# Kernel tuning notes

Hardware: AMD Instinct MI355X
Metric: run time of the kernel (lower is better)

## Reference

```python
import jax, jax.numpy as jnp
import numpy as np


def _lstm(x_seq, W, U, b, h0, c0):
    """Keras-default LSTM. x_seq: [B,T,F]. Gate order i,f,g,o.
    Returns (all hidden states [B,T,H], final h [B,H], final c [B,H])."""
    H = U.shape[0]
    # precompute input projections for all timesteps: [T,B,4H]
    xz = jnp.einsum('btf,fg->tbg', x_seq, W) + b

    def step(carry, xz_t):
        h, c = carry
        z = xz_t + h @ U  # [B,4H]
        i = jax.nn.sigmoid(z[:, 0 * H:1 * H])
        f = jax.nn.sigmoid(z[:, 1 * H:2 * H])
        g = jnp.tanh(z[:, 2 * H:3 * H])
        o = jax.nn.sigmoid(z[:, 3 * H:4 * H])
        c = f * c + i * g
        h = o * jnp.tanh(c)
        return (h, c), h

    (hT, cT), hs = jax.lax.scan(step, (h0, c0), xz)
    return jnp.transpose(hs, (1, 0, 2)), hT, cT  # [B,T,H], [B,H], [B,H]


def setup_inputs() -> dict:
    key = jax.random.key(0)
    ks = jax.random.split(key, 7)
    B, T, F, H, C = 128, 512, 128, 512, 10
    s_in1 = 1.0 / np.sqrt(F)
    s_h = 1.0 / np.sqrt(H)
    return {
        'x': jax.random.normal(ks[0], (B, T, F), jnp.float32),
        'W1': jax.random.normal(ks[1], (F, 4 * H), jnp.float32) * s_in1,
        'U1': jax.random.normal(ks[2], (H, 4 * H), jnp.float32) * s_h,
        'b1': jnp.zeros((4 * H,), jnp.float32),
        'W2': jax.random.normal(ks[3], (H, 4 * H), jnp.float32) * s_h,
        'U2': jax.random.normal(ks[4], (H, 4 * H), jnp.float32) * s_h,
        'b2': jnp.zeros((4 * H,), jnp.float32),
        'Wd': jax.random.normal(ks[5], (H, C), jnp.float32) * s_h,
        'bd': jnp.zeros((C,), jnp.float32),
    }


def reference(x, W1, U1, b1, W2, U2, b2, Wd, bd):
    B = x.shape[0]
    H = U1.shape[0]
    h0 = jnp.zeros((B, H), x.dtype)
    c0 = jnp.zeros((B, H), x.dtype)
    # lstm1: return_sequences + return_state
    seq, h1, c1 = _lstm(x, W1, U1, b1, h0, c0)
    # Keras RNN called on [seq, h, c] uses (h, c) as lstm2's initial state
    _, h2, _ = _lstm(seq, W2, U2, b2, h1, c1)
    logits = h2 @ Wd + bd
    return jax.nn.softmax(logits, axis=-1)
```

## Files before the change

### kernel.cpp

```cpp
#include <hip/hip_runtime.h>
#include <math.h>

#define BB 128
#define TT 512
#define FF 128
#define HH 512
#define NR 2048
#define HB (HH*BB)

typedef __attribute__((ext_vector_type(8))) short short8;
typedef __attribute__((ext_vector_type(4))) float f32x4;
typedef unsigned int uint;
typedef unsigned short ushort;

#define MFMA __builtin_amdgcn_mfma_f32_16x16x32_bf16

__device__ __forceinline__ ushort f2bf(float f) {
  uint u = __float_as_uint(f);
  u += 0x7fff + ((u >> 16) & 1);
  return (ushort)(u >> 16);
}


__global__ __launch_bounds__(256) void k_zero(float* __restrict__ p, int n) {
  int i = blockIdx.x * 256 + threadIdx.x;
  if (i < n) p[i] = 0.f;
}

__global__ __launch_bounds__(256) void k_rearr_b(const float* __restrict__ src,
                                                 float* __restrict__ dst) {
  int idx = blockIdx.x * 256 + threadIdx.x;
  int j = idx & 511, g = idx >> 9;
  dst[j * 4 + g] = src[idx];
}

__global__ __launch_bounds__(256) void k_pack_A(const float* __restrict__ src,
                                                ushort* __restrict__ dst, int ktsh) {
  int idx = blockIdx.x * 256 + threadIdx.x;
  int KTm1 = (1 << ktsh) - 1;
  int j8 = idx & 7;
  int L = (idx >> 3) & 63;
  int kt = (idx >> 9) & KTm1;
  int jb = idx >> (9 + ktsh);
  int k = kt * 32 + (L >> 4) * 8 + j8;
  int m = L & 15;
  int j = jb * 4 + (m >> 2);
  int g = m & 3;
  float v = src[(size_t)k * NR + g * HH + j];
  ushort hi = f2bf(v);
  float fhi = __uint_as_float(((uint)hi) << 16);
  ushort lo = f2bf(v - fhi);
  size_t base = ((size_t)((jb << ktsh) + kt) * 64 + L) * 16;
  dst[base + j8] = hi;
  dst[base + 8 + j8] = lo;
}

__global__ __launch_bounds__(256, 1) void k_fused(
    const float* __restrict__ x,
    const ushort* __restrict__ W1pk, const ushort* __restrict__ U1pk,
    const float* __restrict__ bp1,
    const ushort* __restrict__ W2pk, const ushort* __restrict__ U2pk,
    const float* __restrict__ bp2,
    uint* __restrict__ seq, uint* __restrict__ ring2,
    int* __restrict__ flags) {
  int tid = threadIdx.x;
  int L = tid & 63;
  int ct = tid >> 6;
  int jb = blockIdx.x >> 1;
  int bh = blockIdx.x & 1;
  int q = L >> 4, n = L & 15;
  int col = bh * 64 + ct * 16 + n;
  int j = jb * 4 + q;
  int hrow = q * 8;
  int fi0 = bh * 128 + L;
  int fi1 = fi0 + 64;
  int fme = bh * 128 + jb;

  short8 uh[16], ul[16];
  short8 w1h[4], w1l[4];
  {
    const ushort* ub = U1pk + ((size_t)(jb * 16) * 64 + L) * 16;
#pragma unroll
    for (int kt = 0; kt < 16; ++kt) {
      uh[kt] = *(const short8*)(ub + kt * 1024);
      ul[kt] = *(const short8*)(ub + kt * 1024 + 8);
    }
    const ushort* wb = W1pk + ((size_t)(jb * 4) * 64 + L) * 16;
#pragma unroll
    for (int kt = 0; kt < 4; ++kt) {
      w1h[kt] = *(const short8*)(wb + kt * 1024);
      w1l[kt] = *(const short8*)(wb + kt * 1024 + 8);
    }
  }
  float4 bv = *(const float4*)(bp1 + j * 4);
  float c_reg = 0.f;
  const float* xb = x + (size_t)col * (TT * FF) + hrow;

  f32x4 a0 = {0.f, 0.f, 0.f, 0.f}, a1 = a0, a2 = a0;

#define XPROJ(S) { \
    const float* xp = xb + (size_t)(S) * FF; \
    _Pragma("unroll") \
    for (int kt = 0; kt < 4; ++kt) { \
      float4 v0 = *(const float4*)(xp + kt * 32); \
      float4 v1 = *(const float4*)(xp + kt * 32 + 4); \
      float xf[8] = {v0.x, v0.y, v0.z, v0.w, v1.x, v1.y, v1.z, v1.w}; \
      short8 bhi, blo; \
      _Pragma("unroll") \
      for (int u = 0; u < 8; ++u) { \
        ushort hi = f2bf(xf[u]); \
        blo[u] = (short)f2bf(xf[u] - __uint_as_float(((uint)hi) << 16)); \
        bhi[u] = (short)hi; \
      } \
      a0 = MFMA(w1h[kt], bhi, a0, 0, 0, 0); \
      a1 = MFMA(w1l[kt], bhi, a1, 0, 0, 0); \
      a2 = MFMA(w1h[kt], blo, a2, 0, 0, 0); \
    } }

#define POLL(TGT) { \
    while (true) { \
      int f0 = __hip_atomic_load(&flags[fi0], __ATOMIC_RELAXED, __HIP_MEMORY_SCOPE_AGENT); \
      int f1 = __hip_atomic_load(&flags[fi1], __ATOMIC_RELAXED, __HIP_MEMORY_SCOPE_AGENT); \
      if (__all((f0 >= (TGT)) && (f1 >= (TGT)))) break; \
    } \
    asm volatile("" ::: "memory"); }

  XPROJ(0)
#pragma unroll 1
  for (int s = 0; s < TT; ++s) {
    if (s > 0) {
      POLL(s)
      const uint* hc = seq + (size_t)(s - 1) * HB + (size_t)hrow * BB + col;
      uint w[16][8];
#pragma unroll
      for (int kt = 0; kt < 16; ++kt)
#pragma unroll
        for (int u = 0; u < 8; ++u)
          w[kt][u] = hc[(size_t)(kt * 32 + u) * BB];
#pragma unroll
      for (int kt = 0; kt < 16; ++kt) {
        short8 bhi, blo;
#pragma unroll
        for (int u = 0; u < 8; ++u) {
          bhi[u] = (short)(w[kt][u] >> 16);
          blo[u] = (short)(w[kt][u] & 0xffffu);
        }
        a0 = MFMA(uh[kt], bhi, a0, 0, 0, 0);
        a1 = MFMA(ul[kt], bhi, a1, 0, 0, 0);
        a2 = MFMA(uh[kt], blo, a2, 0, 0, 0);
      }
    }
    float z0 = a0.x + a1.x + a2.x + bv.x;
    float z1 = a0.y + a1.y + a2.y + bv.y;
    float z2 = a0.z + a1.z + a2.z + bv.z;
    float z3 = a0.w + a1.w + a2.w + bv.w;
    float ig = 1.f / (1.f + __expf(-z0));
    float fg = 1.f / (1.f + __expf(-z1));
    float gg = tanhf(z2);
    float og = 1.f / (1.f + __expf(-z3));
    c_reg = fg * c_reg + ig * gg;
    float hn = og * tanhf(c_reg);
    ushort hi = f2bf(hn);
    uint word = (((uint)hi) << 16) |
                (uint)f2bf(hn - __uint_as_float(((uint)hi) << 16));
    __hip_atomic_store(&seq[(size_t)s * HB + (size_t)j * BB + col], word,
                       __ATOMIC_RELAXED, __HIP_MEMORY_SCOPE_AGENT);
    if (s == TT - 1)
      __hip_atomic_store(&ring2[(size_t)3 * HB + (size_t)j * BB + col], word,
                         __ATOMIC_RELAXED, __HIP_MEMORY_SCOPE_AGENT);
    __syncthreads();
    if (tid == 0)
      __hip_atomic_store(&flags[fme], s + 1, __ATOMIC_RELAXED,
                         __HIP_MEMORY_SCOPE_AGENT);
    a0 = (f32x4){0.f, 0.f, 0.f, 0.f}; a1 = a0; a2 = a0;
    if (s + 1 < TT) XPROJ(s + 1)
  }

  {
    const ushort* ub = U2pk + ((size_t)(jb * 16) * 64 + L) * 16;
#pragma unroll
    for (int kt = 0; kt < 16; ++kt) {
      uh[kt] = *(const short8*)(ub + kt * 1024);
      ul[kt] = *(const short8*)(ub + kt * 1024 + 8);
    }
  }
  bv = *(const float4*)(bp2 + j * 4);
  const ushort* w2b = W2pk + ((size_t)(jb * 16) * 64 + L) * 16;

#define G1PROJ(S) { \
    const uint* h1c = seq + (size_t)(S) * HB + (size_t)hrow * BB + col; \
    uint w[16][8]; \
    _Pragma("unroll") \
    for (int kt = 0; kt < 16; ++kt) \
      _Pragma("unroll") \
      for (int u = 0; u < 8; ++u) \
        w[kt][u] = h1c[(size_t)(kt * 32 + u) * BB]; \
    _Pragma("unroll") \
    for (int kt = 0; kt < 16; ++kt) { \
      short8 w2h = *(const short8*)(w2b + kt * 1024); \
      short8 w2l = *(const short8*)(w2b + kt * 1024 + 8); \
      short8 bhi, blo; \
      _Pragma("unroll") \
      for (int u = 0; u < 8; ++u) { \
        bhi[u] = (short)(w[kt][u] >> 16); \
        blo[u] = (short)(w[kt][u] & 0xffffu); \
      } \
      a0 = MFMA(w2h, bhi, a0, 0, 0, 0); \
      a1 = MFMA(w2l, bhi, a1, 0, 0, 0); \
      a2 = MFMA(w2h, blo, a2, 0, 0, 0); \
    } }

  G1PROJ(0)
#pragma unroll 1
  for (int s = 0; s < TT; ++s) {
    POLL(TT + s)
    {
      const uint* hc = ring2 + (size_t)((s + 3) & 3) * HB + (size_t)hrow * BB + col;
      uint w[16][8];
#pragma unroll
      for (int kt = 0; kt < 16; ++kt)
#pragma unroll
        for (int u = 0; u < 8; ++u)
          w[kt][u] = __hip_atomic_load(&hc[(size_t)(kt * 32 + u) * BB],
                                       __ATOMIC_RELAXED, __HIP_MEMORY_SCOPE_AGENT);
#pragma unroll
      for (int kt = 0; kt < 16; ++kt) {
        short8 bhi, blo;
#pragma unroll
        for (int u = 0; u < 8; ++u) {
          bhi[u] = (short)(w[kt][u] >> 16);
          blo[u] = (short)(w[kt][u] & 0xffffu);
        }
        a0 = MFMA(uh[kt], bhi, a0, 0, 0, 0);
        a1 = MFMA(ul[kt], bhi, a1, 0, 0, 0);
        a2 = MFMA(uh[kt], blo, a2, 0, 0, 0);
      }
    }
    float z0 = a0.x + a1.x + a2.x + bv.x;
    float z1 = a0.y + a1.y + a2.y + bv.y;
    float z2 = a0.z + a1.z + a2.z + bv.z;
    float z3 = a0.w + a1.w + a2.w + bv.w;
    float ig = 1.f / (1.f + __expf(-z0));
    float fg = 1.f / (1.f + __expf(-z1));
    float gg = tanhf(z2);
    float og = 1.f / (1.f + __expf(-z3));
    c_reg = fg * c_reg + ig * gg;
    float hn = og * tanhf(c_reg);
    ushort hi = f2bf(hn);
    uint word = (((uint)hi) << 16) |
                (uint)f2bf(hn - __uint_as_float(((uint)hi) << 16));
    __hip_atomic_store(&ring2[(size_t)(s & 3) * HB + (size_t)j * BB + col], word,
                       __ATOMIC_RELAXED, __HIP_MEMORY_SCOPE_AGENT);
    __syncthreads();
    if (tid == 0)
      __hip_atomic_store(&flags[fme], TT + s + 1, __ATOMIC_RELAXED,
                         __HIP_MEMORY_SCOPE_AGENT);
    a0 = (f32x4){0.f, 0.f, 0.f, 0.f}; a1 = a0; a2 = a0;
    if (s + 1 < TT) G1PROJ(s + 1)
  }
}

__global__ __launch_bounds__(64) void k_dense(const uint* __restrict__ h2,
                                              const float* __restrict__ Wd,
                                              const float* __restrict__ bd,
                                              float* __restrict__ out) {
  int b = blockIdx.x * 64 + threadIdx.x;
  float acc[10];
#pragma unroll
  for (int c = 0; c < 10; ++c) acc[c] = bd[c];
  for (int k = 0; k < HH; ++k) {
    uint w = h2[k * BB + b];
    float hv = __uint_as_float(w & 0xffff0000u) + __uint_as_float(w << 16);
#pragma unroll
    for (int c = 0; c < 10; ++c) acc[c] = fmaf(hv, Wd[k * 10 + c], acc[c]);
  }
  float m = acc[0];
#pragma unroll
  for (int c = 1; c < 10; ++c) m = fmaxf(m, acc[c]);
  float s = 0.f;
#pragma unroll
  for (int c = 0; c < 10; ++c) { acc[c] = __expf(acc[c] - m); s += acc[c]; }
  float inv = 1.f / s;
#pragma unroll
  for (int c = 0; c < 10; ++c) out[b * 10 + c] = acc[c] * inv;
}

extern "C" void kernel_launch(void* const* d_in, const int* in_sizes, int n_in,
                              void* d_out, int out_size, void* d_ws, size_t ws_size,
                              hipStream_t stream) {
  const float* x  = (const float*)d_in[0];
  const float* W1 = (const float*)d_in[1];
  const float* U1 = (const float*)d_in[2];
  const float* b1 = (const float*)d_in[3];
  const float* W2 = (const float*)d_in[4];
  const float* U2 = (const float*)d_in[5];
  const float* b2 = (const float*)d_in[6];
  const float* Wd = (const float*)d_in[7];
  const float* bd = (const float*)d_in[8];
  float* out = (float*)d_out;

  uint*   seq   = (uint*)d_ws;
  uint*   ring2 = seq + (size_t)TT * HB;
  float*  bp1   = (float*)(ring2 + (size_t)4 * HB);
  float*  bp2   = bp1 + NR;
  ushort* W1pk  = (ushort*)(bp2 + NR);
  ushort* U1pk  = W1pk + (size_t)524288;
  ushort* U2pk  = U1pk + (size_t)2097152;
  ushort* W2pk  = U2pk + (size_t)2097152;
  int*    flags = (int*)(W2pk + (size_t)2097152);

  k_zero<<<1, 256, 0, stream>>>((float*)flags, 256);
  k_rearr_b<<<NR / 256, 256, 0, stream>>>(b1, bp1);
  k_rearr_b<<<NR / 256, 256, 0, stream>>>(b2, bp2);
  k_pack_A<<<1024, 256, 0, stream>>>(W1, W1pk, 2);
  k_pack_A<<<4096, 256, 0, stream>>>(U1, U1pk, 4);
  k_pack_A<<<4096, 256, 0, stream>>>(U2, U2pk, 4);
  k_pack_A<<<4096, 256, 0, stream>>>(W2, W2pk, 4);

  k_fused<<<256, 256, 0, stream>>>(x, W1pk, U1pk, bp1, W2pk, U2pk, bp2,
                                   seq, ring2, flags);
  k_dense<<<BB / 64, 64, 0, stream>>>(ring2 + (size_t)3 * HB, Wd, bd, out);
}
```

Measured before the change: 5.088 ms.

## Split persistent LSTM kernel into recurrent and input-projection block roles

The 256 persistent blocks are split into two roles. 128 recurrent blocks each own two hidden-row tiles for 32 batch columns and run only the h@U recurrence across both layers. The other 128 blocks compute the input projections (x@W1, then h1@W2) up to four steps ahead into a ring buffer, with producer/consumer flags padded onto separate cache lines. The hidden state is now stored as separate hi/lo bf16 planes in batch-major layout, so operand fetches are contiguous 16-byte loads instead of strided 32-bit gathers. This takes the projection work off the serial critical path, at the cost of holding twice as many U registers per recurrent block and adding a second synchronisation channel.

Measured after the change: 8.399 ms. 65.1% more time.

```diff
diff --git a/kernel.cpp b/kernel.cpp
--- a/kernel.cpp
+++ b/kernel.cpp
@@ -7,18 +7,29 @@
 #define HH 512
 #define NR 2048
 #define HB (HH*BB)
+#define FLS 16
 
 typedef __attribute__((ext_vector_type(8))) short short8;
 typedef __attribute__((ext_vector_type(4))) float f32x4;
 typedef unsigned int uint;
 typedef unsigned short ushort;
+typedef unsigned long long u64;
 
 #define MFMA __builtin_amdgcn_mfma_f32_16x16x32_bf16
+#define AT_LD(p)   __hip_atomic_load((p), __ATOMIC_RELAXED, __HIP_MEMORY_SCOPE_AGENT)
+#define AT_ST(p,v) __hip_atomic_store((p), (v), __ATOMIC_RELAXED, __HIP_MEMORY_SCOPE_AGENT)
 
 __device__ __forceinline__ ushort f2bf(float f) {
   uint u = __float_as_uint(f);
   u += 0x7fff + ((u >> 16) & 1);
   return (ushort)(u >> 16);
+}
+__device__ __forceinline__ float bfh(ushort h) { return __uint_as_float(((uint)h) << 16); }
+__device__ __forceinline__ void st2_wt(ushort* p, uint v) {
+  asm volatile("global_store_short %0, %1, off sc0 sc1" :: "v"(p), "v"(v) : "memory");
+}
+__device__ __forceinline__ u64 pk2f(float a, float b) {
+  return ((u64)__float_as_uint(b) << 32) | (u64)__float_as_uint(a);
 }
 
 
@@ -48,8 +59,7 @@
   int g = m & 3;
   float v = src[(size_t)k * NR + g * HH + j];
   ushort hi = f2bf(v);
-  float fhi = __uint_as_float(((uint)hi) << 16);
-  ushort lo = f2bf(v - fhi);
+  ushort lo = f2bf(v - bfh(hi));
   size_t base = ((size_t)((jb << ktsh) + kt) * 64 + L) * 16;
   dst[base + j8] = hi;
   dst[base + 8 + j8] = lo;
@@ -61,206 +71,234 @@
     const float* __restrict__ bp1,
     const ushort* __restrict__ W2pk, const ushort* __restrict__ U2pk,
     const float* __restrict__ bp2,
-    uint* __restrict__ seq, uint* __restrict__ ring2,
-    int* __restrict__ flags) {
+    ushort* __restrict__ shi, ushort* __restrict__ slo,
+    ushort* __restrict__ rhi, ushort* __restrict__ rlo,
+    float4* __restrict__ xzr,
+    int* __restrict__ hflags, int* __restrict__ pflags) {
   int tid = threadIdx.x;
   int L = tid & 63;
-  int ct = tid >> 6;
-  int jb = blockIdx.x >> 1;
-  int bh = blockIdx.x & 1;
+  int w = tid >> 6;
   int q = L >> 4, n = L & 15;
-  int col = bh * 64 + ct * 16 + n;
-  int j = jb * 4 + q;
-  int hrow = q * 8;
-  int fi0 = bh * 128 + L;
-  int fi1 = fi0 + 64;
-  int fme = bh * 128 + jb;
-
-  short8 uh[16], ul[16];
-  short8 w1h[4], w1l[4];
-  {
-    const ushort* ub = U1pk + ((size_t)(jb * 16) * 64 + L) * 16;
-#pragma unroll
-    for (int kt = 0; kt < 16; ++kt) {
-      uh[kt] = *(const short8*)(ub + kt * 1024);
-      ul[kt] = *(const short8*)(ub + kt * 1024 + 8);
+  int rtp = w & 1, ctw = w >> 1;
+  bool isrec = (blockIdx.x < 128);
+  int b = isrec ? blockIdx.x : (blockIdx.x - 128);
+  int ch = b & 3, jb2 = b >> 2;
+  int col = ch * 32 + ctw * 16 + n;
+  int jbp0 = jb2 * 4 + rtp * 2;
+  int j0 = jbp0 * 4 + q;
+
+  if (isrec) {
+    short8 uh[2][16], ul[2][16];
+    auto loadU = [&](const ushort* Up) {
+#pragma unroll
+      for (int r = 0; r < 2; ++r)
+#pragma unroll
+        for (int kt = 0; kt < 16; ++kt) {
+          const ushort* p = Up + (((size_t)(jbp0 + r) * 16 + kt) * 64 + L) * 16;
+          uh[r][kt] = *(const short8*)(p);
+          ul[r][kt] = *(const short8*)(p + 8);
+        }
+    };
+    loadU(U1pk);
+    float4 bv[2];
+    bv[0] = *(const float4*)(bp1 + j0 * 4);
+    bv[1] = *(const float4*)(bp1 + (j0 + 4) * 4);
+    float c_reg[2] = {0.f, 0.f};
+    int fidx = ((L & 31) * 4 + ch) * FLS;
+
+#pragma unroll 1
+    for (int G = 0; G < 2 * TT; ++G) {
+      if (G == TT) {
+        loadU(U2pk);
+        bv[0] = *(const float4*)(bp2 + j0 * 4);
+        bv[1] = *(const float4*)(bp2 + (j0 + 4) * 4);
+      }
+      while (true) {
+        int hf = AT_LD(hflags + fidx);
+        int pf = AT_LD(pflags + b * FLS);
+        if (__all((hf >= G) && (pf >= G + 1))) break;
+      }
+      asm volatile("" ::: "memory");
+      float xzv[2][4];
+#pragma unroll
+      for (int r = 0; r < 2; ++r) {
+        const u64* xp = (const u64*)(xzr + ((size_t)(G & 3) * HB + (j0 + 4 * r) * BB + col));
+        u64 a = AT_LD(xp), bq = AT_LD(xp + 1);
+        xzv[r][0] = __uint_as_float((uint)a);
+        xzv[r][1] = __uint_as_float((uint)(a >> 32));
+        xzv[r][2] = __uint_as_float((uint)bq);
+        xzv[r][3] = __uint_as_float((uint)(bq >> 32));
+      }
+      f32x4 A0[2], A1[2], A2[2];
+#pragma unroll
+      for (int r = 0; r < 2; ++r) {
+        A0[r] = (f32x4){0.f, 0.f, 0.f, 0.f}; A1[r] = A0[r]; A2[r] = A0[r];
+      }
+      if (G != 0) {
+        if (G < TT) {
+          const ushort* ph = shi + (size_t)(G - 1) * HB + (size_t)col * HH + q * 8;
+          const ushort* pl = slo + (size_t)(G - 1) * HB + (size_t)col * HH + q * 8;
+#pragma unroll
+          for (int kh = 0; kh < 2; ++kh) {
+            short8 bh[8], bl[8];
+#pragma unroll
+            for (int k8 = 0; k8 < 8; ++k8) {
+              bh[k8] = *(const short8*)(ph + (kh * 8 + k8) * 32);
+              bl[k8] = *(const short8*)(pl + (kh * 8 + k8) * 32);
+            }
+#pragma unroll
+            for (int k8 = 0; k8 < 8; ++k8) {
+              int kt = kh * 8 + k8;
+#pragma unroll
+              for (int r = 0; r < 2; ++r) {
+                A0[r] = MFMA(uh[r][kt], bh[k8], A0[r], 0, 0, 0);
+                A1[r] = MFMA(ul[r][kt], bh[k8], A1[r], 0, 0, 0);
+                A2[r] = MFMA(uh[r][kt], bl[k8], A2[r], 0, 0, 0);
+              }
+            }
+          }
+        } else {
+          size_t rb = (size_t)((G - 1) & 3) * HB + (size_t)col * HH + q * 8;
+          const u64* ph = (const u64*)(rhi + rb);
+          const u64* pl = (const u64*)(rlo + rb);
+#pragma unroll
+          for (int kh = 0; kh < 2; ++kh) {
+            short8 bh[8], bl[8];
+#pragma unroll
+            for (int k8 = 0; k8 < 8; ++k8) {
+              int kt = kh * 8 + k8;
+              union { short8 v; u64 u[2]; } fh, fl;
+              fh.u[0] = AT_LD(ph + kt * 8); fh.u[1] = AT_LD(ph + kt * 8 + 1);
+              fl.u[0] = AT_LD(pl + kt * 8); fl.u[1] = AT_LD(pl + kt * 8 + 1);
+              bh[k8] = fh.v; bl[k8] = fl.v;
+            }
+#pragma unroll
+            for (int k8 = 0; k8 < 8; ++k8) {
+              int kt = kh * 8 + k8;
+#pragma unroll
+              for (int r = 0; r < 2; ++r) {
+                A0[r] = MFMA(uh[r][kt], bh[k8], A0[r], 0, 0, 0);
+                A1[r] = MFMA(ul[r][kt], bh[k8], A1[r], 0, 0, 0);
+                A2[r] = MFMA(uh[r][kt], bl[k8], A2[r], 0, 0, 0);
+              }
+            }
+          }
+        }
+      }
+#pragma unroll
+      for (int r = 0; r < 2; ++r) {
+        float z0 = A0[r].x + A1[r].x + A2[r].x + xzv[r][0];
+        float z1 = A0[r].y + A1[r].y + A2[r].y + xzv[r][1];
+        float z2 = A0[r].z + A1[r].z + A2[r].z + xzv[r][2];
+        float z3 = A0[r].w + A1[r].w + A2[r].w + xzv[r][3];
+        float ig = 1.f / (1.f + __expf(-z0));
+        float fg = 1.f / (1.f + __expf(-z1));
+        float gg = tanhf(z2);
+        float og = 1.f / (1.f + __expf(-z3));
+        c_reg[r] = fg * c_reg[r] + ig * gg;
+        float hn = og * tanhf(c_reg[r]);
+        ushort hh = f2bf(hn);
+        ushort hl = f2bf(hn - bfh(hh));
+        size_t off = (size_t)col * HH + (j0 + 4 * r);
+        if (G < TT) {
+          st2_wt(shi + (size_t)G * HB + off, hh);
+          st2_wt(slo + (size_t)G * HB + off, hl);
+        }
+        if (G >= TT - 1) {
+          st2_wt(rhi + (size_t)(G & 3) * HB + off, hh);
+          st2_wt(rlo + (size_t)(G & 3) * HB + off, hl);
+        }
+      }
+      __syncthreads();
+      if (tid == 0) AT_ST(hflags + b * FLS, G + 1);
     }
-    const ushort* wb = W1pk + ((size_t)(jb * 4) * 64 + L) * 16;
-#pragma unroll
-    for (int kt = 0; kt < 4; ++kt) {
-      w1h[kt] = *(const short8*)(wb + kt * 1024);
-      w1l[kt] = *(const short8*)(wb + kt * 1024 + 8);
+  } else {
+    short8 w1h[2][4], w1l[2][4];
+#pragma unroll
+    for (int r = 0; r < 2; ++r)
+#pragma unroll
+      for (int kt = 0; kt < 4; ++kt) {
+        const ushort* p = W1pk + (((size_t)(jbp0 + r) * 4 + kt) * 64 + L) * 16;
+        w1h[r][kt] = *(const short8*)(p);
+        w1l[r][kt] = *(const short8*)(p + 8);
+      }
+    float4 bv[2];
+    bv[0] = *(const float4*)(bp1 + j0 * 4);
+    bv[1] = *(const float4*)(bp1 + (j0 + 4) * 4);
+
+#pragma unroll 1
+    for (int G = 0; G < 2 * TT; ++G) {
+      if (G == TT) {
+        bv[0] = *(const float4*)(bp2 + j0 * 4);
+        bv[1] = *(const float4*)(bp2 + (j0 + 4) * 4);
+      }
+      if (G >= 4) {
+        while (AT_LD(hflags + b * FLS) < G - 3) {}
+      }
+      asm volatile("" ::: "memory");
+      f32x4 P0[2], P1[2], P2[2];
+#pragma unroll
+      for (int r = 0; r < 2; ++r) {
+        P0[r] = (f32x4){0.f, 0.f, 0.f, 0.f}; P1[r] = P0[r]; P2[r] = P0[r];
+      }
+      if (G < TT) {
+        const float* xp = x + ((size_t)col * TT + G) * FF + q * 8;
+#pragma unroll
+        for (int kt = 0; kt < 4; ++kt) {
+          float4 v0 = *(const float4*)(xp + kt * 32);
+          float4 v1 = *(const float4*)(xp + kt * 32 + 4);
+          float xf[8] = {v0.x, v0.y, v0.z, v0.w, v1.x, v1.y, v1.z, v1.w};
+          short8 xh, xl;
+#pragma unroll
+          for (int u = 0; u < 8; ++u) {
+            ushort hi = f2bf(xf[u]);
+            xl[u] = (short)f2bf(xf[u] - bfh(hi));
+            xh[u] = (short)hi;
+          }
+#pragma unroll
+          for (int r = 0; r < 2; ++r) {
+            P0[r] = MFMA(w1h[r][kt], xh, P0[r], 0, 0, 0);
+            P1[r] = MFMA(w1l[r][kt], xh, P1[r], 0, 0, 0);
+            P2[r] = MFMA(w1h[r][kt], xl, P2[r], 0, 0, 0);
+          }
+        }
+      } else {
+        int sp = G - TT;
+        const ushort* ph = shi + (size_t)sp * HB + (size_t)col * HH + q * 8;
+        const ushort* pl = slo + (size_t)sp * HB + (size_t)col * HH + q * 8;
+#pragma unroll
+        for (int kt = 0; kt < 16; ++kt) {
+          short8 bh = *(const short8*)(ph + kt * 32);
+          short8 bl = *(const short8*)(pl + kt * 32);
+#pragma unroll
+          for (int r = 0; r < 2; ++r) {
+            const ushort* ab = W2pk + (((size_t)(jbp0 + r) * 16 + kt) * 64 + L) * 16;
+            short8 ah = *(const short8*)(ab);
+            short8 al = *(const short8*)(ab + 8);
+            P0[r] = MFMA(ah, bh, P0[r], 0, 0, 0);
+            P1[r] = MFMA(al, bh, P1[r], 0, 0, 0);
+            P2[r] = MFMA(ah, bl, P2[r], 0, 0, 0);
+          }
+        }
+      }
+#pragma unroll
+      for (int r = 0; r < 2; ++r) {
+        float o0 = P0[r].x + P1[r].x + P2[r].x + bv[r].x;
+        float o1 = P0[r].y + P1[r].y + P2[r].y + bv[r].y;
+        float o2 = P0[r].z + P1[r].z + P2[r].z + bv[r].z;
+        float o3 = P0[r].w + P1[r].w + P2[r].w + bv[r].w;
+        u64* dp = (u64*)(xzr + ((size_t)(G & 3) * HB + (j0 + 4 * r) * BB + col));
+        AT_ST(dp, pk2f(o0, o1));
+        AT_ST(dp + 1, pk2f(o2, o3));
+      }
+      __syncthreads();
+      if (tid == 0) AT_ST(pflags + b * FLS, G + 1);
     }
   }
-  float4 bv = *(const float4*)(bp1 + j * 4);
-  float c_reg = 0.f;
-  const float* xb = x + (size_t)col * (TT * FF) + hrow;
-
-  f32x4 a0 = {0.f, 0.f, 0.f, 0.f}, a1 = a0, a2 = a0;
-
-#define XPROJ(S) { \
-    const float* xp = xb + (size_t)(S) * FF; \
-    _Pragma("unroll") \
-    for (int kt = 0; kt < 4; ++kt) { \
-      float4 v0 = *(const float4*)(xp + kt * 32); \
-      float4 v1 = *(const float4*)(xp + kt * 32 + 4); \
-      float xf[8] = {v0.x, v0.y, v0.z, v0.w, v1.x, v1.y, v1.z, v1.w}; \
-      short8 bhi, blo; \
-      _Pragma("unroll") \
-      for (int u = 0; u < 8; ++u) { \
-        ushort hi = f2bf(xf[u]); \
-        blo[u] = (short)f2bf(xf[u] - __uint_as_float(((uint)hi) << 16)); \
-        bhi[u] = (short)hi; \
-      } \
-      a0 = MFMA(w1h[kt], bhi, a0, 0, 0, 0); \
-      a1 = MFMA(w1l[kt], bhi, a1, 0, 0, 0); \
-      a2 = MFMA(w1h[kt], blo, a2, 0, 0, 0); \
-    } }
-
-#define POLL(TGT) { \
-    while (true) { \
-      int f0 = __hip_atomic_load(&flags[fi0], __ATOMIC_RELAXED, __HIP_MEMORY_SCOPE_AGENT); \
-      int f1 = __hip_atomic_load(&flags[fi1], __ATOMIC_RELAXED, __HIP_MEMORY_SCOPE_AGENT); \
-      if (__all((f0 >= (TGT)) && (f1 >= (TGT)))) break; \
-    } \
-    asm volatile("" ::: "memory"); }
-
-  XPROJ(0)
-#pragma unroll 1
-  for (int s = 0; s < TT; ++s) {
-    if (s > 0) {
-      POLL(s)
-      const uint* hc = seq + (size_t)(s - 1) * HB + (size_t)hrow * BB + col;
-      uint w[16][8];
-#pragma unroll
-      for (int kt = 0; kt < 16; ++kt)
-#pragma unroll
-        for (int u = 0; u < 8; ++u)
-          w[kt][u] = hc[(size_t)(kt * 32 + u) * BB];
-#pragma unroll
-      for (int kt = 0; kt < 16; ++kt) {
-        short8 bhi, blo;
-#pragma unroll
-        for (int u = 0; u < 8; ++u) {
-          bhi[u] = (short)(w[kt][u] >> 16);
-          blo[u] = (short)(w[kt][u] & 0xffffu);
-        }
-        a0 = MFMA(uh[kt], bhi, a0, 0, 0, 0);
-        a1 = MFMA(ul[kt], bhi, a1, 0, 0, 0);
-        a2 = MFMA(uh[kt], blo, a2, 0, 0, 0);
-      }
-    }
-    float z0 = a0.x + a1.x + a2.x + bv.x;
-    float z1 = a0.y + a1.y + a2.y + bv.y;
-    float z2 = a0.z + a1.z + a2.z + bv.z;
-    float z3 = a0.w + a1.w + a2.w + bv.w;
-    float ig = 1.f / (1.f + __expf(-z0));
-    float fg = 1.f / (1.f + __expf(-z1));
-    float gg = tanhf(z2);
-    float og = 1.f / (1.f + __expf(-z3));
-    c_reg = fg * c_reg + ig * gg;
-    float hn = og * tanhf(c_reg);
-    ushort hi = f2bf(hn);
-    uint word = (((uint)hi) << 16) |
-                (uint)f2bf(hn - __uint_as_float(((uint)hi) << 16));
-    __hip_atomic_store(&seq[(size_t)s * HB + (size_t)j * BB + col], word,
-                       __ATOMIC_RELAXED, __HIP_MEMORY_SCOPE_AGENT);
-    if (s == TT - 1)
-      __hip_atomic_store(&ring2[(size_t)3 * HB + (size_t)j * BB + col], word,
-                         __ATOMIC_RELAXED, __HIP_MEMORY_SCOPE_AGENT);
-    __syncthreads();
-    if (tid == 0)
-      __hip_atomic_store(&flags[fme], s + 1, __ATOMIC_RELAXED,
-                         __HIP_MEMORY_SCOPE_AGENT);
-    a0 = (f32x4){0.f, 0.f, 0.f, 0.f}; a1 = a0; a2 = a0;
-    if (s + 1 < TT) XPROJ(s + 1)
-  }
-
-  {
-    const ushort* ub = U2pk + ((size_t)(jb * 16) * 64 + L) * 16;
-#pragma unroll
-    for (int kt = 0; kt < 16; ++kt) {
-      uh[kt] = *(const short8*)(ub + kt * 1024);
-      ul[kt] = *(const short8*)(ub + kt * 1024 + 8);
-    }
-  }
-  bv = *(const float4*)(bp2 + j * 4);
-  const ushort* w2b = W2pk + ((size_t)(jb * 16) * 64 + L) * 16;
-
-#define G1PROJ(S) { \
-    const uint* h1c = seq + (size_t)(S) * HB + (size_t)hrow * BB + col; \
-    uint w[16][8]; \
-    _Pragma("unroll") \
-    for (int kt = 0; kt < 16; ++kt) \
-      _Pragma("unroll") \
-      for (int u = 0; u < 8; ++u) \
-        w[kt][u] = h1c[(size_t)(kt * 32 + u) * BB]; \
-    _Pragma("unroll") \
-    for (int kt = 0; kt < 16; ++kt) { \
-      short8 w2h = *(const short8*)(w2b + kt * 1024); \
-      short8 w2l = *(const short8*)(w2b + kt * 1024 + 8); \
-      short8 bhi, blo; \
-      _Pragma("unroll") \
-      for (int u = 0; u < 8; ++u) { \
-        bhi[u] = (short)(w[kt][u] >> 16); \
-        blo[u] = (short)(w[kt][u] & 0xffffu); \
-      } \
-      a0 = MFMA(w2h, bhi, a0, 0, 0, 0); \
-      a1 = MFMA(w2l, bhi, a1, 0, 0, 0); \
-      a2 = MFMA(w2h, blo, a2, 0, 0, 0); \
-    } }
-
-  G1PROJ(0)
-#pragma unroll 1
-  for (int s = 0; s < TT; ++s) {
-    POLL(TT + s)
-    {
-      const uint* hc = ring2 + (size_t)((s + 3) & 3) * HB + (size_t)hrow * BB + col;
-      uint w[16][8];
-#pragma unroll
-      for (int kt = 0; kt < 16; ++kt)
-#pragma unroll
-        for (int u = 0; u < 8; ++u)
-          w[kt][u] = __hip_atomic_load(&hc[(size_t)(kt * 32 + u) * BB],
-                                       __ATOMIC_RELAXED, __HIP_MEMORY_SCOPE_AGENT);
-#pragma unroll
-      for (int kt = 0; kt < 16; ++kt) {
-        short8 bhi, blo;
-#pragma unroll
-        for (int u = 0; u < 8; ++u) {
-          bhi[u] = (short)(w[kt][u] >> 16);
-          blo[u] = (short)(w[kt][u] & 0xffffu);
-        }
-        a0 = MFMA(uh[kt], bhi, a0, 0, 0, 0);
-        a1 = MFMA(ul[kt], bhi, a1, 0, 0, 0);
-        a2 = MFMA(uh[kt], blo, a2, 0, 0, 0);
-      }
-    }
-    float z0 = a0.x + a1.x + a2.x + bv.x;
-    float z1 = a0.y + a1.y + a2.y + bv.y;
-    float z2 = a0.z + a1.z + a2.z + bv.z;
-    float z3 = a0.w + a1.w + a2.w + bv.w;
-    float ig = 1.f / (1.f + __expf(-z0));
-    float fg = 1.f / (1.f + __expf(-z1));
-    float gg = tanhf(z2);
-    float og = 1.f / (1.f + __expf(-z3));
-    c_reg = fg * c_reg + ig * gg;
-    float hn = og * tanhf(c_reg);
-    ushort hi = f2bf(hn);
-    uint word = (((uint)hi) << 16) |
-                (uint)f2bf(hn - __uint_as_float(((uint)hi) << 16));
-    __hip_atomic_store(&ring2[(size_t)(s & 3) * HB + (size_t)j * BB + col], word,
-                       __ATOMIC_RELAXED, __HIP_MEMORY_SCOPE_AGENT);
-    __syncthreads();
-    if (tid == 0)
-      __hip_atomic_store(&flags[fme], TT + s + 1, __ATOMIC_RELAXED,
-                         __HIP_MEMORY_SCOPE_AGENT);
-    a0 = (f32x4){0.f, 0.f, 0.f, 0.f}; a1 = a0; a2 = a0;
-    if (s + 1 < TT) G1PROJ(s + 1)
-  }
-}
-
-__global__ __launch_bounds__(64) void k_dense(const uint* __restrict__ h2,
+}
+
+__global__ __launch_bounds__(64) void k_dense(const ushort* __restrict__ rhi,
+                                              const ushort* __restrict__ rlo,
                                               const float* __restrict__ Wd,
                                               const float* __restrict__ bd,
                                               float* __restrict__ out) {
@@ -268,9 +306,10 @@
   float acc[10];
 #pragma unroll
   for (int c = 0; c < 10; ++c) acc[c] = bd[c];
+  const ushort* ph = rhi + (size_t)3 * HB + (size_t)b * HH;
+  const ushort* pl = rlo + (size_t)3 * HB + (size_t)b * HH;
   for (int k = 0; k < HH; ++k) {
-    uint w = h2[k * BB + b];
-    float hv = __uint_as_float(w & 0xffff0000u) + __uint_as_float(w << 16);
+    float hv = bfh(ph[k]) + bfh(pl[k]);
 #pragma unroll
     for (int c = 0; c < 10; ++c) acc[c] = fmaf(hv, Wd[k * 10 + c], acc[c]);
   }
@@ -299,25 +338,29 @@
   const float* bd = (const float*)d_in[8];
   float* out = (float*)d_out;
 
-  uint*   seq   = (uint*)d_ws;
-  uint*   ring2 = seq + (size_t)TT * HB;
-  float*  bp1   = (float*)(ring2 + (size_t)4 * HB);
-  float*  bp2   = bp1 + NR;
-  ushort* W1pk  = (ushort*)(bp2 + NR);
+  ushort* shi   = (ushort*)d_ws;
+  ushort* slo   = shi + (size_t)TT * HB;
+  ushort* rhi   = slo + (size_t)TT * HB;
+  ushort* rlo   = rhi + (size_t)4 * HB;
+  float4* xzr   = (float4*)(rlo + (size_t)4 * HB);
+  ushort* W1pk  = (ushort*)(xzr + (size_t)4 * HB);
   ushort* U1pk  = W1pk + (size_t)524288;
   ushort* U2pk  = U1pk + (size_t)2097152;
   ushort* W2pk  = U2pk + (size_t)2097152;
-  int*    flags = (int*)(W2pk + (size_t)2097152);
-
-  k_zero<<<1, 256, 0, stream>>>((float*)flags, 256);
-  k_rearr_b<<<NR / 256, 256, 0, stream>>>(b1, bp1);
-  k_rearr_b<<<NR / 256, 256, 0, stream>>>(b2, bp2);
+  float*  bp1   = (float*)(W2pk + (size_t)2097152);
+  float*  bp2   = bp1 + NR;
+  int*    hflags = (int*)(bp2 + NR);
+  int*    pflags = hflags + 128 * FLS;
+
+  k_zero<<<16, 256, 0, stream>>>((float*)hflags, 2 * 128 * FLS);
+  k_rearr_b<<<8, 256, 0, stream>>>(b1, bp1);
+  k_rearr_b<<<8, 256, 0, stream>>>(b2, bp2);
   k_pack_A<<<1024, 256, 0, stream>>>(W1, W1pk, 2);
   k_pack_A<<<4096, 256, 0, stream>>>(U1, U1pk, 4);
   k_pack_A<<<4096, 256, 0, stream>>>(U2, U2pk, 4);
   k_pack_A<<<4096, 256, 0, stream>>>(W2, W2pk, 4);
 
   k_fused<<<256, 256, 0, stream>>>(x, W1pk, U1pk, bp1, W2pk, U2pk, bp2,
-                                   seq, ring2, flags);
-  k_dense<<<BB / 64, 64, 0, stream>>>(ring2 + (size_t)3 * HB, Wd, bd, out);
-}
+                                   shi, slo, rhi, rlo, xzr, hflags, pflags);
+  k_dense<<<2, 64, 0, stream>>>(rhi, rlo, Wd, bd, out);
+}
```
